# Kernel tuning notes

Measured on AMD Instinct MI355X. Metric: run time of the kernel, lower is better.

The kernel has to match this reference:

```python
import jax, jax.numpy as jnp
import numpy as np
from jax.ops import segment_sum

N_USERS = 100_000
N_ITEMS = 200_000
D = 64
NNZ = 5_000_000
GNN_LAYERS = 2


def setup_inputs() -> dict:
    key = jax.random.key(0)
    k0, k1, k2, k3, k4 = jax.random.split(key, 5)
    # Embedding tables (xavier-ish scale)
    user_emb = jax.random.normal(k0, (N_USERS, D), jnp.float32) * 0.1
    item_emb = jax.random.normal(k1, (N_ITEMS, D), jnp.float32) * 0.1
    # Sparse normalized bipartite adjacency adj_norm [n_users, n_items] in COO form
    adj_vals = jax.random.uniform(k2, (NNZ,), jnp.float32)
    adj_rows = jax.random.randint(k3, (NNZ,), 0, N_USERS, jnp.int32)
    adj_cols = jax.random.randint(k4, (NNZ,), 0, N_ITEMS, jnp.int32)
    return {
        "user_emb": user_emb,
        "item_emb": item_emb,
        "adj_vals": adj_vals,
        "adj_rows": adj_rows,
        "adj_cols": adj_cols,
    }


def reference(user_emb, item_emb, adj_vals, adj_rows, adj_cols):
    """Student_LightGCL.forward with is_test=True.

    NormLayer with mode 'None' is identity. Then gnn_layer rounds of
    bipartite sparse propagation:
      Z_u = adj_norm   @ E_i   (spmm -> gather + segment_sum over users)
      Z_i = adj_norm.T @ E_u
    Output: mean over layer-0..L embeddings for users and items.
    """
    E_u, E_i = user_emb, item_emb
    sum_u, sum_i = E_u, E_i
    for _ in range(GNN_LAYERS):
        # Z_u[r] = sum_{e: rows[e]==r} vals[e] * E_i[cols[e]]
        Z_u = segment_sum(adj_vals[:, None] * E_i[adj_cols], adj_rows,
                          num_segments=N_USERS)
        Z_i = segment_sum(adj_vals[:, None] * E_u[adj_rows], adj_cols,
                          num_segments=N_ITEMS)
        E_u, E_i = Z_u, Z_i
        sum_u = sum_u + E_u
        sum_i = sum_i + E_i
    inv = 1.0 / (GNN_LAYERS + 1)
    return sum_u * inv, sum_i * inv
```

## Files before the change

kernel.cpp:

```cpp
#include <hip/hip_runtime.h>


constexpr int D = 64;
constexpr int RPB = 64;
constexpr int ACC = 32;
constexpr int NBMAX = 5120;
constexpr int REF_CAP = 4000;
constexpr int PASSB_EDGES = 8192;

static __device__ __forceinline__ unsigned short f32_to_bf16(float f) {
    unsigned u = __float_as_uint(f);
    unsigned r = u + 0x7FFFu + ((u >> 16) & 1u);
    return (unsigned short)(r >> 16);
}
static __device__ __forceinline__ float bf16_lo(unsigned g) {
    return __uint_as_float(g << 16);
}
static __device__ __forceinline__ float bf16_hi(unsigned g) {
    return __uint_as_float(g & 0xFFFF0000u);
}


__global__ __launch_bounds__(1024) void bucket_hist(
    const int* __restrict__ rows, const int* __restrict__ cols,
    int* __restrict__ bktCnt, int nu, int nnz, int NB) {
    __shared__ int cnt[NBMAX];
    for (int i = threadIdx.x; i < NB; i += blockDim.x) cnt[i] = 0;
    __syncthreads();
    int stride = gridDim.x * blockDim.x;
    for (int e = blockIdx.x * blockDim.x + threadIdx.x; e < nnz; e += stride) {
        atomicAdd(&cnt[rows[e] >> 6], 1);
        atomicAdd(&cnt[(nu + cols[e]) >> 6], 1);
    }
    __syncthreads();
    for (int i = threadIdx.x; i < NB; i += blockDim.x)
        if (cnt[i]) atomicAdd(&bktCnt[i], cnt[i]);
}

__global__ void scan_buckets(const int* __restrict__ bktCnt,
                             int* __restrict__ bktBase, int* __restrict__ bktCur,
                             int NB, int total) {
    __shared__ int tsum[256];
    int t = threadIdx.x;
    const int IT = (NB + 255) / 256;
    int v[20];
    int s = 0;
    for (int k = 0; k < IT; k++) {
        int i = t * IT + k;
        v[k] = (i < NB) ? bktCnt[i] : 0;
        s += v[k];
    }
    tsum[t] = s;
    __syncthreads();
    for (int off = 1; off < 256; off <<= 1) {
        int x = (t >= off) ? tsum[t - off] : 0;
        __syncthreads();
        tsum[t] += x;
        __syncthreads();
    }
    int excl = (t > 0) ? tsum[t - 1] : 0;
    for (int k = 0; k < IT; k++) {
        int i = t * IT + k;
        if (i < NB) { bktBase[i] = excl; bktCur[i] = excl; excl += v[k]; }
    }
    if (t == 255) bktBase[NB] = total;
}

__global__ __launch_bounds__(512) void pass_bucket(
    const float* __restrict__ vals, const int* __restrict__ rows,
    const int* __restrict__ cols, int* __restrict__ bktCur,
    int2* __restrict__ tmp, int nu, int nnz, int NB) {
    __shared__ int cnt[NBMAX];
    for (int i = threadIdx.x; i < NB; i += 512) cnt[i] = 0;
    __syncthreads();
    int base = blockIdx.x * PASSB_EDGES;
    for (int k = 0; k < PASSB_EDGES / 512; k++) {
        int e = base + k * 512 + threadIdx.x;
        if (e < nnz) {
            atomicAdd(&cnt[rows[e] >> 6], 1);
            atomicAdd(&cnt[(nu + cols[e]) >> 6], 1);
        }
    }
    __syncthreads();
    for (int i = threadIdx.x; i < NB; i += 512) {
        int c = cnt[i];
        if (c) cnt[i] = atomicAdd(&bktCur[i], c);
    }
    __syncthreads();
    for (int k = 0; k < PASSB_EDGES / 512; k++) {
        int e = base + k * 512 + threadIdx.x;
        if (e < nnz) {
            int r = rows[e], c = cols[e];
            int iv = __float_as_int(vals[e]);
            int gi = nu + c;
            int p1 = atomicAdd(&cnt[r >> 6], 1);
            tmp[p1] = make_int2(((r & 63) << 19) | gi, iv);
            int p2 = atomicAdd(&cnt[gi >> 6], 1);
            tmp[p2] = make_int2(((gi & 63) << 19) | r, iv);
        }
    }
}

__global__ __launch_bounds__(512) void refine_kernel(
    int2* __restrict__ tmp, const int* __restrict__ bktBase,
    int* __restrict__ rowStart, int NB) {
    __shared__ int2 stage[REF_CAP];
    __shared__ int h[RPB], cur[RPB];
    int b = blockIdx.x;
    int beg = bktBase[b], end = bktBase[b + 1];
    int n = end - beg;
    int t = threadIdx.x;
    if (t == 0 && b == NB - 1) rowStart[(size_t)NB * RPB] = end;
    if (t < RPB) h[t] = 0;
    __syncthreads();
    if (n <= REF_CAP) {
        for (int e = t; e < n; e += 512) {
            int2 v = tmp[beg + e];
            stage[e] = v;
            atomicAdd(&h[(v.x >> 19) & (RPB - 1)], 1);
        }
        __syncthreads();
        int myc = (t < RPB) ? h[t] : 0;
        for (int off = 1; off < RPB; off <<= 1) {
            int x = 0;
            if (t < RPB && t >= off) x = h[t - off];
            __syncthreads();
            if (t < RPB) h[t] += x;
            __syncthreads();
        }
        if (t < RPB) {
            int excl = beg + h[t] - myc;
            cur[t] = excl;
            rowStart[(size_t)b * RPB + t] = excl;
        }
        __syncthreads();
        for (int e = t; e < n; e += 512) {
            int2 v = stage[e];
            int p = atomicAdd(&cur[(v.x >> 19) & (RPB - 1)], 1);
            tmp[p] = v;
        }
    } else {
        if (t < RPB) rowStart[(size_t)b * RPB + t] = (t == 0) ? -(beg + 1) : 0;
    }
}

__global__ void convert_e0(const float* __restrict__ Eu,
                           const float* __restrict__ Ei,
                           unsigned short* __restrict__ Ecat,
                           long long nuD, long long nD) {
    long long stride = (long long)gridDim.x * blockDim.x * 4;
    for (long long i = ((long long)blockIdx.x * blockDim.x + threadIdx.x) * 4;
         i < nD; i += stride) {
        const float* src = (i < nuD) ? (Eu + i) : (Ei + (i - nuD));
        float4 f = *(const float4*)src;
        unsigned short o0 = f32_to_bf16(f.x), o1 = f32_to_bf16(f.y);
        unsigned short o2 = f32_to_bf16(f.z), o3 = f32_to_bf16(f.w);
        *(uint2*)(Ecat + i) =
            make_uint2(((unsigned)o1 << 16) | o0, ((unsigned)o3 << 16) | o2);
    }
}

template <bool FUSE>
__global__ __launch_bounds__(256, 8) void accum7_kernel(
    const int2* __restrict__ tmp, const int* __restrict__ bktBase,
    const int* __restrict__ rowStart,
    const unsigned short* __restrict__ gsrc,
    const float* __restrict__ Eu0, const float* __restrict__ Ei0,
    const unsigned short* __restrict__ Z1,
    unsigned short* __restrict__ Zout,
    float* __restrict__ out,
    int nu, int nR) {
    int b = blockIdx.x;
    int w = threadIdx.x >> 6, lane = threadIdx.x & 63;
    int q = lane >> 4, m = lane & 15;
    int rb64 = (b * ACC) >> 6;
    int bEnd = bktBase[rb64 + 1];
    int rb0 = rowStart[(size_t)rb64 << 6];
    bool sorted = (rb0 >= 0);
    const uint2* gp = (const uint2*)gsrc + m;

    for (int k = 0; k < 8; k += 2) {
        int grA = b * ACC + (w << 3) + k;
        if (grA >= nR) break;
        bool hasB = (grA + 1) < nR;

        float a0 = 0.f, a1 = 0.f, a2 = 0.f, a3 = 0.f;
        float b0 = 0.f, b1 = 0.f, b2 = 0.f, b3 = 0.f;

        if (sorted) {
            int eA0 = rowStart[grA], eA1 = rowStart[grA + 1];
            int eB0 = eA1;
            int eB1 = hasB ? (((grA & 63) == 62) ? bEnd : rowStart[grA + 2])
                           : eB0;
            int nA = eA1 - eA0, nB = eB1 - eB0;
            int iters = ((nA > nB ? nA : nB) + 3) >> 2;
            int eA = eA0 + q, eB = eB0 + q;

            int2 sAc = tmp[eA], sBc = tmp[eB];
            int2 sAn = tmp[eA + 4], sBn = tmp[eB + 4];
            bool okA = eA < eA1, okB = eB < eB1;
            uint2 gAc = gp[(okA ? (sAc.x & 0x7FFFF) : 0) << 4];
            uint2 gBc = gp[(okB ? (sBc.x & 0x7FFFF) : 0) << 4];
            float vAc = okA ? __int_as_float(sAc.y) : 0.f;
            float vBc = okB ? __int_as_float(sBc.y) : 0.f;

            for (int i = 0; i < iters; i++) {
                int2 sAn2 = tmp[eA + 8];
                int2 sBn2 = tmp[eB + 8];
                bool okA1 = (eA + 4) < eA1;
                bool okB1 = (eB + 4) < eB1;
                uint2 gAn = gp[(okA1 ? (sAn.x & 0x7FFFF) : 0) << 4];
                uint2 gBn = gp[(okB1 ? (sBn.x & 0x7FFFF) : 0) << 4];
                float vAn = okA1 ? __int_as_float(sAn.y) : 0.f;
                float vBn = okB1 ? __int_as_float(sBn.y) : 0.f;

                a0 += vAc * bf16_lo(gAc.x); a1 += vAc * bf16_hi(gAc.x);
                a2 += vAc * bf16_lo(gAc.y); a3 += vAc * bf16_hi(gAc.y);
                b0 += vBc * bf16_lo(gBc.x); b1 += vBc * bf16_hi(gBc.x);
                b2 += vBc * bf16_lo(gBc.y); b3 += vBc * bf16_hi(gBc.y);

                sAn = sAn2; sBn = sBn2;
                gAc = gAn;  gBc = gBn;
                vAc = vAn;  vBc = vBn;
                eA += 4; eB += 4;
            }
        } else {
            int beg = -(rb0 + 1);
            int n = bEnd - beg;
            int iters = (n + 3) >> 2;
            int e = beg + q;
            int rlA = grA & 63;
            for (int i = 0; i < iters; i++) {
                int2 s = tmp[e];
                int rl = (s.x >> 19) & 63;
                bool in = e < bEnd;
                bool okA = in && (rl == rlA);
                bool okB = in && hasB && (rl == rlA + 1);
                int rx = (okA | okB) ? (s.x & 0x7FFFF) : 0;
                float vA = okA ? __int_as_float(s.y) : 0.f;
                float vB = okB ? __int_as_float(s.y) : 0.f;
                uint2 g = gp[rx << 4];
                a0 += vA * bf16_lo(g.x); a1 += vA * bf16_hi(g.x);
                a2 += vA * bf16_lo(g.y); a3 += vA * bf16_hi(g.y);
                b0 += vB * bf16_lo(g.x); b1 += vB * bf16_hi(g.x);
                b2 += vB * bf16_lo(g.y); b3 += vB * bf16_hi(g.y);
                e += 4;
            }
        }

        a0 += __shfl_xor(a0, 16, 64); a0 += __shfl_xor(a0, 32, 64);
        a1 += __shfl_xor(a1, 16, 64); a1 += __shfl_xor(a1, 32, 64);
        a2 += __shfl_xor(a2, 16, 64); a2 += __shfl_xor(a2, 32, 64);
        a3 += __shfl_xor(a3, 16, 64); a3 += __shfl_xor(a3, 32, 64);
        b0 += __shfl_xor(b0, 16, 64); b0 += __shfl_xor(b0, 32, 64);
        b1 += __shfl_xor(b1, 16, 64); b1 += __shfl_xor(b1, 32, 64);
        b2 += __shfl_xor(b2, 16, 64); b2 += __shfl_xor(b2, 32, 64);
        b3 += __shfl_xor(b3, 16, 64); b3 += __shfl_xor(b3, 32, 64);

        int wr = (q == 0) ? grA : ((q == 1 && hasB) ? grA + 1 : -1);
        if (wr >= 0) {
            float r0 = (q == 0) ? a0 : b0;
            float r1 = (q == 0) ? a1 : b1;
            float r2 = (q == 0) ? a2 : b2;
            float r3 = (q == 0) ? a3 : b3;
            long long o = (long long)wr * D + m * 4;
            if (!FUSE) {
                unsigned p0 = ((unsigned)f32_to_bf16(r1) << 16) | f32_to_bf16(r0);
                unsigned p1 = ((unsigned)f32_to_bf16(r3) << 16) | f32_to_bf16(r2);
                *(uint2*)(Zout + o) = make_uint2(p0, p1);
            } else {
                const float* e0p = (wr < nu)
                    ? (Eu0 + o) : (Ei0 + o - (long long)nu * D);
                float4 e0 = *(const float4*)e0p;
                uint2 z = *(const uint2*)(Z1 + o);
                const float inv3 = 1.f / 3.f;
                float4 ov;
                ov.x = (e0.x + bf16_lo(z.x) + r0) * inv3;
                ov.y = (e0.y + bf16_hi(z.x) + r1) * inv3;
                ov.z = (e0.z + bf16_lo(z.y) + r2) * inv3;
                ov.w = (e0.w + bf16_hi(z.y) + r3) * inv3;
                *(float4*)(out + o) = ov;
            }
        }
    }
}


__global__ void spmm_edge(const float* __restrict__ vals,
                          const int* __restrict__ rows,
                          const int* __restrict__ cols,
                          const float* __restrict__ Eu,
                          const float* __restrict__ Ei,
                          float* __restrict__ Zu, float* __restrict__ Zi,
                          float scale, int nnz) {
    long long gid = (long long)blockIdx.x * blockDim.x + threadIdx.x;
    if (gid >= (long long)nnz * D) return;
    int e = (int)(gid >> 6);
    int d = (int)(gid & 63);
    float v = vals[e] * scale;
    long long r = rows[e];
    long long c = cols[e];
    atomicAdd(&Zu[r * D + d], v * Ei[c * D + d]);
    atomicAdd(&Zi[c * D + d], v * Eu[r * D + d]);
}

__global__ void combine_kernel(const float* __restrict__ E0,
                               const float* __restrict__ Z1,
                               float* __restrict__ out, long long n4) {
    long long i = (long long)blockIdx.x * blockDim.x + threadIdx.x;
    if (i >= n4) return;
    const float4 a = reinterpret_cast<const float4*>(E0)[i];
    const float4 b = reinterpret_cast<const float4*>(Z1)[i];
    const float inv3 = 1.0f / 3.0f;
    float4 o;
    o.x = (a.x + b.x) * inv3;
    o.y = (a.y + b.y) * inv3;
    o.z = (a.z + b.z) * inv3;
    o.w = (a.w + b.w) * inv3;
    reinterpret_cast<float4*>(out)[i] = o;
}


static inline size_t align256(size_t x) { return (x + 255) & ~(size_t)255; }

extern "C" void kernel_launch(void* const* d_in, const int* in_sizes, int n_in,
                              void* d_out, int out_size, void* d_ws, size_t ws_size,
                              hipStream_t stream) {
    const float* user_emb = (const float*)d_in[0];
    const float* item_emb = (const float*)d_in[1];
    const float* vals     = (const float*)d_in[2];
    const int*   rows     = (const int*)d_in[3];
    const int*   cols     = (const int*)d_in[4];

    const int nu  = in_sizes[0] / D;
    const int ni  = in_sizes[1] / D;
    const int nnz = in_sizes[2];
    const int nR  = nu + ni;
    const int NB  = (nR + RPB - 1) / RPB;

    float* out = (float*)d_out;

    size_t off = 0;
    size_t o_tmp  = off; off += align256(((size_t)2 * nnz + 32) * sizeof(int2));
    size_t o_E    = off; off += align256((size_t)nR * D * sizeof(unsigned short));
    size_t o_Z1   = off; off += align256((size_t)nR * D * sizeof(unsigned short));
    size_t o_cnt  = off; off += align256((size_t)(NB + 1) * sizeof(int));
    size_t o_base = off; off += align256((size_t)(NB + 2) * sizeof(int));
    size_t o_cur  = off; off += align256((size_t)(NB + 1) * sizeof(int));
    size_t o_row  = off; off += align256(((size_t)NB * RPB + 1) * sizeof(int));
    size_t needed = off;

    bool fits19 = (nR < (1 << 19));

    if (ws_size >= needed && NB <= NBMAX && fits19) {
        char* w = (char*)d_ws;
        int2*           tmp      = (int2*)(w + o_tmp);
        unsigned short* Ecat     = (unsigned short*)(w + o_E);
        unsigned short* Z1bf     = (unsigned short*)(w + o_Z1);
        int*            bktCnt   = (int*)(w + o_cnt);
        int*            bktBase  = (int*)(w + o_base);
        int*            bktCur   = (int*)(w + o_cur);
        int*            rowStart = (int*)(w + o_row);

        hipMemsetAsync(bktCnt, 0, (size_t)NB * sizeof(int), stream);

        bucket_hist<<<512, 1024, 0, stream>>>(rows, cols, bktCnt, nu, nnz, NB);
        scan_buckets<<<1, 256, 0, stream>>>(bktCnt, bktBase, bktCur, NB, 2 * nnz);

        unsigned gB = (unsigned)((nnz + PASSB_EDGES - 1) / PASSB_EDGES);
        pass_bucket<<<gB, 512, 0, stream>>>(vals, rows, cols, bktCur, tmp,
                                            nu, nnz, NB);
        refine_kernel<<<NB, 512, 0, stream>>>(tmp, bktBase, rowStart, NB);

        long long nD = (long long)nR * D;
        long long nuD = (long long)nu * D;
        unsigned gC = (unsigned)((nD / 4 + 255) / 256);
        if (gC > 4096) gC = 4096;
        convert_e0<<<gC, 256, 0, stream>>>(user_emb, item_emb, Ecat, nuD, nD);

        unsigned gA = (unsigned)((nR + ACC - 1) / ACC);
        accum7_kernel<false><<<gA, 256, 0, stream>>>(
            tmp, bktBase, rowStart, Ecat, nullptr, nullptr, nullptr, Z1bf,
            nullptr, nu, nR);
        accum7_kernel<true><<<gA, 256, 0, stream>>>(
            tmp, bktBase, rowStart, Z1bf, user_emb, item_emb, Z1bf, nullptr,
            out, nu, nR);
    } else {
        float* Zu1 = (float*)d_ws;
        float* Zi1 = Zu1 + (size_t)nu * D;
        float* out_u = out;
        float* out_i = out + (size_t)nu * D;
        hipMemsetAsync(d_ws, 0, (size_t)nR * D * sizeof(float), stream);

        const int threads = 256;
        long long tot = (long long)nnz * D;
        unsigned blocks = (unsigned)((tot + threads - 1) / threads);

        spmm_edge<<<blocks, threads, 0, stream>>>(vals, rows, cols, user_emb,
                                                  item_emb, Zu1, Zi1, 1.0f, nnz);
        long long nu4 = (long long)nu * D / 4;
        long long ni4 = (long long)ni * D / 4;
        combine_kernel<<<(unsigned)((nu4 + 255) / 256), 256, 0, stream>>>(
            user_emb, Zu1, out_u, nu4);
        combine_kernel<<<(unsigned)((ni4 + 255) / 256), 256, 0, stream>>>(
            item_emb, Zi1, out_i, ni4);
        spmm_edge<<<blocks, threads, 0, stream>>>(vals, rows, cols, Zu1, Zi1,
                                                  out_u, out_i, 1.0f / 3.0f, nnz);
    }
}
```

Before: 780.4 us.

## Fuse per-bucket refine sort with first-layer SpMM accumulation from shared memory

The separate refine kernel is folded into a new accum_sort_l1 kernel. It sorts each 64-row bucket in shared memory using an index permutation, writes the sorted edges back for layer 2, and computes the layer-1 aggregation directly from the staged edges instead of re-reading them from global memory in a separate launch. pass_bucket also moves from 512 to 1024 threads per block. The costs are one fewer launch and one fewer global read of the edge list, traded against heavier per-block shared memory use (lower occupancy) and 512-thread blocks doing the gather work.

```diff
diff --git a/kernel.cpp b/kernel.cpp
--- a/kernel.cpp
+++ b/kernel.cpp
@@ -66,29 +66,29 @@
     if (t == 255) bktBase[NB] = total;
 }
 
-__global__ __launch_bounds__(512) void pass_bucket(
+__global__ __launch_bounds__(1024) void pass_bucket(
     const float* __restrict__ vals, const int* __restrict__ rows,
     const int* __restrict__ cols, int* __restrict__ bktCur,
     int2* __restrict__ tmp, int nu, int nnz, int NB) {
     __shared__ int cnt[NBMAX];
-    for (int i = threadIdx.x; i < NB; i += 512) cnt[i] = 0;
+    for (int i = threadIdx.x; i < NB; i += 1024) cnt[i] = 0;
     __syncthreads();
     int base = blockIdx.x * PASSB_EDGES;
-    for (int k = 0; k < PASSB_EDGES / 512; k++) {
-        int e = base + k * 512 + threadIdx.x;
+    for (int k = 0; k < PASSB_EDGES / 1024; k++) {
+        int e = base + k * 1024 + threadIdx.x;
         if (e < nnz) {
             atomicAdd(&cnt[rows[e] >> 6], 1);
             atomicAdd(&cnt[(nu + cols[e]) >> 6], 1);
         }
     }
     __syncthreads();
-    for (int i = threadIdx.x; i < NB; i += 512) {
+    for (int i = threadIdx.x; i < NB; i += 1024) {
         int c = cnt[i];
         if (c) cnt[i] = atomicAdd(&bktCur[i], c);
     }
     __syncthreads();
-    for (int k = 0; k < PASSB_EDGES / 512; k++) {
-        int e = base + k * 512 + threadIdx.x;
+    for (int k = 0; k < PASSB_EDGES / 1024; k++) {
+        int e = base + k * 1024 + threadIdx.x;
         if (e < nnz) {
             int r = rows[e], c = cols[e];
             int iv = __float_as_int(vals[e]);
@@ -98,49 +98,6 @@
             int p2 = atomicAdd(&cnt[gi >> 6], 1);
             tmp[p2] = make_int2(((gi & 63) << 19) | r, iv);
         }
-    }
-}
-
-__global__ __launch_bounds__(512) void refine_kernel(
-    int2* __restrict__ tmp, const int* __restrict__ bktBase,
-    int* __restrict__ rowStart, int NB) {
-    __shared__ int2 stage[REF_CAP];
-    __shared__ int h[RPB], cur[RPB];
-    int b = blockIdx.x;
-    int beg = bktBase[b], end = bktBase[b + 1];
-    int n = end - beg;
-    int t = threadIdx.x;
-    if (t == 0 && b == NB - 1) rowStart[(size_t)NB * RPB] = end;
-    if (t < RPB) h[t] = 0;
-    __syncthreads();
-    if (n <= REF_CAP) {
-        for (int e = t; e < n; e += 512) {
-            int2 v = tmp[beg + e];
-            stage[e] = v;
-            atomicAdd(&h[(v.x >> 19) & (RPB - 1)], 1);
-        }
-        __syncthreads();
-        int myc = (t < RPB) ? h[t] : 0;
-        for (int off = 1; off < RPB; off <<= 1) {
-            int x = 0;
-            if (t < RPB && t >= off) x = h[t - off];
-            __syncthreads();
-            if (t < RPB) h[t] += x;
-            __syncthreads();
-        }
-        if (t < RPB) {
-            int excl = beg + h[t] - myc;
-            cur[t] = excl;
-            rowStart[(size_t)b * RPB + t] = excl;
-        }
-        __syncthreads();
-        for (int e = t; e < n; e += 512) {
-            int2 v = stage[e];
-            int p = atomicAdd(&cur[(v.x >> 19) & (RPB - 1)], 1);
-            tmp[p] = v;
-        }
-    } else {
-        if (t < RPB) rowStart[(size_t)b * RPB + t] = (t == 0) ? -(beg + 1) : 0;
     }
 }
 
@@ -160,14 +117,175 @@
     }
 }
 
-template <bool FUSE>
+__global__ __launch_bounds__(512) void accum_sort_l1(
+    int2* __restrict__ tmp, const int* __restrict__ bktBase,
+    int* __restrict__ rowStart,
+    const unsigned short* __restrict__ gsrc,
+    unsigned short* __restrict__ Zout,
+    int nu, int nR) {
+    __shared__ int2 stage[REF_CAP];
+    __shared__ unsigned short idx[REF_CAP];
+    __shared__ int h[RPB], cur[RPB], rs[RPB + 1];
+    int b = blockIdx.x;
+    int beg = bktBase[b], end = bktBase[b + 1];
+    int n = end - beg;
+    int t = threadIdx.x;
+    if (t < RPB) h[t] = 0;
+    if (t == 0) { stage[0] = make_int2(0, 0); idx[0] = 0; }
+    __syncthreads();
+
+    int w = t >> 6, lane = t & 63;
+    int q = lane >> 4, m = lane & 15;
+    const uint2* gp = (const uint2*)gsrc + m;
+
+    if (n <= REF_CAP) {
+        for (int e = t; e < n; e += 512) {
+            int2 v = tmp[beg + e];
+            stage[e] = v;
+            atomicAdd(&h[(v.x >> 19) & (RPB - 1)], 1);
+        }
+        __syncthreads();
+        int myc = (t < RPB) ? h[t] : 0;
+        for (int off = 1; off < RPB; off <<= 1) {
+            int x = 0;
+            if (t < RPB && t >= off) x = h[t - off];
+            __syncthreads();
+            if (t < RPB) h[t] += x;
+            __syncthreads();
+        }
+        if (t < RPB) {
+            int excl = h[t] - myc;
+            cur[t] = excl;
+            rs[t] = excl;
+            rowStart[(size_t)b * RPB + t] = beg + excl;
+        }
+        if (t == 0) rs[RPB] = n;
+        __syncthreads();
+        for (int e = t; e < n; e += 512) {
+            int2 v = stage[e];
+            int p = atomicAdd(&cur[(v.x >> 19) & (RPB - 1)], 1);
+            idx[p] = (unsigned short)e;
+        }
+        __syncthreads();
+        for (int e = t; e < n; e += 512) tmp[beg + e] = stage[idx[e]];
+
+        for (int k = 0; k < 8; k += 2) {
+            int rlA = (w << 3) + k;
+            int grA = b * RPB + rlA;
+            if (grA >= nR) break;
+            bool hasB = (grA + 1) < nR;
+            int eA0 = rs[rlA], eA1 = rs[rlA + 1];
+            int eB0 = eA1;
+            int eB1 = hasB ? rs[rlA + 2] : eA1;
+            int nA = eA1 - eA0, nB = eB1 - eB0;
+            int iters = ((nA > nB ? nA : nB) + 3) >> 2;
+
+            float a0 = 0.f, a1 = 0.f, a2 = 0.f, a3 = 0.f;
+            float b0 = 0.f, b1 = 0.f, b2 = 0.f, b3 = 0.f;
+            int eA = eA0 + q, eB = eB0 + q;
+
+            bool okA = eA < eA1, okB = eB < eB1;
+            int2 sA = stage[idx[okA ? eA : 0]];
+            int2 sB = stage[idx[okB ? eB : 0]];
+            uint2 gA = gp[(okA ? (sA.x & 0x7FFFF) : 0) << 4];
+            uint2 gB = gp[(okB ? (sB.x & 0x7FFFF) : 0) << 4];
+            float vA = okA ? __int_as_float(sA.y) : 0.f;
+            float vB = okB ? __int_as_float(sB.y) : 0.f;
+
+            for (int i = 0; i < iters; i++) {
+                bool okA1 = (eA + 4) < eA1, okB1 = (eB + 4) < eB1;
+                int2 sAn = stage[idx[okA1 ? eA + 4 : 0]];
+                int2 sBn = stage[idx[okB1 ? eB + 4 : 0]];
+
+                a0 += vA * bf16_lo(gA.x); a1 += vA * bf16_hi(gA.x);
+                a2 += vA * bf16_lo(gA.y); a3 += vA * bf16_hi(gA.y);
+                b0 += vB * bf16_lo(gB.x); b1 += vB * bf16_hi(gB.x);
+                b2 += vB * bf16_lo(gB.y); b3 += vB * bf16_hi(gB.y);
+
+                gA = gp[(okA1 ? (sAn.x & 0x7FFFF) : 0) << 4];
+                gB = gp[(okB1 ? (sBn.x & 0x7FFFF) : 0) << 4];
+                vA = okA1 ? __int_as_float(sAn.y) : 0.f;
+                vB = okB1 ? __int_as_float(sBn.y) : 0.f;
+                eA += 4; eB += 4;
+            }
+
+            a0 += __shfl_xor(a0, 16, 64); a0 += __shfl_xor(a0, 32, 64);
+            a1 += __shfl_xor(a1, 16, 64); a1 += __shfl_xor(a1, 32, 64);
+            a2 += __shfl_xor(a2, 16, 64); a2 += __shfl_xor(a2, 32, 64);
+            a3 += __shfl_xor(a3, 16, 64); a3 += __shfl_xor(a3, 32, 64);
+            b0 += __shfl_xor(b0, 16, 64); b0 += __shfl_xor(b0, 32, 64);
+            b1 += __shfl_xor(b1, 16, 64); b1 += __shfl_xor(b1, 32, 64);
+            b2 += __shfl_xor(b2, 16, 64); b2 += __shfl_xor(b2, 32, 64);
+            b3 += __shfl_xor(b3, 16, 64); b3 += __shfl_xor(b3, 32, 64);
+
+            int wr = (q == 0) ? grA : ((q == 1 && hasB) ? grA + 1 : -1);
+            if (wr >= 0) {
+                float r0 = (q == 0) ? a0 : b0;
+                float r1 = (q == 0) ? a1 : b1;
+                float r2 = (q == 0) ? a2 : b2;
+                float r3 = (q == 0) ? a3 : b3;
+                long long o = (long long)wr * D + m * 4;
+                unsigned p0 = ((unsigned)f32_to_bf16(r1) << 16) | f32_to_bf16(r0);
+                unsigned p1 = ((unsigned)f32_to_bf16(r3) << 16) | f32_to_bf16(r2);
+                *(uint2*)(Zout + o) = make_uint2(p0, p1);
+            }
+        }
+    } else {
+        if (t < RPB) rowStart[(size_t)b * RPB + t] = (t == 0) ? -(beg + 1) : 0;
+        __syncthreads();
+        for (int k = 0; k < 8; k += 2) {
+            int rlA = (w << 3) + k;
+            int grA = b * RPB + rlA;
+            if (grA >= nR) break;
+            bool hasB = (grA + 1) < nR;
+            float a0 = 0.f, a1 = 0.f, a2 = 0.f, a3 = 0.f;
+            float b0 = 0.f, b1 = 0.f, b2 = 0.f, b3 = 0.f;
+            int iters = (n + 3) >> 2;
+            int e = beg + q;
+            for (int i = 0; i < iters; i++) {
+                int2 s = (e < end) ? tmp[e] : make_int2(0, 0);
+                int rl = (s.x >> 19) & (RPB - 1);
+                bool okA = (e < end) && (rl == rlA);
+                bool okB = (e < end) && hasB && (rl == rlA + 1);
+                int rx = (okA | okB) ? (s.x & 0x7FFFF) : 0;
+                float vA = okA ? __int_as_float(s.y) : 0.f;
+                float vB = okB ? __int_as_float(s.y) : 0.f;
+                uint2 g = gp[rx << 4];
+                a0 += vA * bf16_lo(g.x); a1 += vA * bf16_hi(g.x);
+                a2 += vA * bf16_lo(g.y); a3 += vA * bf16_hi(g.y);
+                b0 += vB * bf16_lo(g.x); b1 += vB * bf16_hi(g.x);
+                b2 += vB * bf16_lo(g.y); b3 += vB * bf16_hi(g.y);
+                e += 4;
+            }
+            a0 += __shfl_xor(a0, 16, 64); a0 += __shfl_xor(a0, 32, 64);
+            a1 += __shfl_xor(a1, 16, 64); a1 += __shfl_xor(a1, 32, 64);
+            a2 += __shfl_xor(a2, 16, 64); a2 += __shfl_xor(a2, 32, 64);
+            a3 += __shfl_xor(a3, 16, 64); a3 += __shfl_xor(a3, 32, 64);
+            b0 += __shfl_xor(b0, 16, 64); b0 += __shfl_xor(b0, 32, 64);
+            b1 += __shfl_xor(b1, 16, 64); b1 += __shfl_xor(b1, 32, 64);
+            b2 += __shfl_xor(b2, 16, 64); b2 += __shfl_xor(b2, 32, 64);
+            b3 += __shfl_xor(b3, 16, 64); b3 += __shfl_xor(b3, 32, 64);
+            int wr = (q == 0) ? grA : ((q == 1 && hasB) ? grA + 1 : -1);
+            if (wr >= 0) {
+                float r0 = (q == 0) ? a0 : b0;
+                float r1 = (q == 0) ? a1 : b1;
+                float r2 = (q == 0) ? a2 : b2;
+                float r3 = (q == 0) ? a3 : b3;
+                long long o = (long long)wr * D + m * 4;
+                unsigned p0 = ((unsigned)f32_to_bf16(r1) << 16) | f32_to_bf16(r0);
+                unsigned p1 = ((unsigned)f32_to_bf16(r3) << 16) | f32_to_bf16(r2);
+                *(uint2*)(Zout + o) = make_uint2(p0, p1);
+            }
+        }
+    }
+}
+
 __global__ __launch_bounds__(256, 8) void accum7_kernel(
     const int2* __restrict__ tmp, const int* __restrict__ bktBase,
     const int* __restrict__ rowStart,
     const unsigned short* __restrict__ gsrc,
     const float* __restrict__ Eu0, const float* __restrict__ Ei0,
     const unsigned short* __restrict__ Z1,
-    unsigned short* __restrict__ Zout,
     float* __restrict__ out,
     int nu, int nR) {
     int b = blockIdx.x;
@@ -264,23 +382,17 @@
             float r2 = (q == 0) ? a2 : b2;
             float r3 = (q == 0) ? a3 : b3;
             long long o = (long long)wr * D + m * 4;
-            if (!FUSE) {
-                unsigned p0 = ((unsigned)f32_to_bf16(r1) << 16) | f32_to_bf16(r0);
-                unsigned p1 = ((unsigned)f32_to_bf16(r3) << 16) | f32_to_bf16(r2);
-                *(uint2*)(Zout + o) = make_uint2(p0, p1);
-            } else {
-                const float* e0p = (wr < nu)
-                    ? (Eu0 + o) : (Ei0 + o - (long long)nu * D);
-                float4 e0 = *(const float4*)e0p;
-                uint2 z = *(const uint2*)(Z1 + o);
-                const float inv3 = 1.f / 3.f;
-                float4 ov;
-                ov.x = (e0.x + bf16_lo(z.x) + r0) * inv3;
-                ov.y = (e0.y + bf16_hi(z.x) + r1) * inv3;
-                ov.z = (e0.z + bf16_lo(z.y) + r2) * inv3;
-                ov.w = (e0.w + bf16_hi(z.y) + r3) * inv3;
-                *(float4*)(out + o) = ov;
-            }
+            const float* e0p = (wr < nu)
+                ? (Eu0 + o) : (Ei0 + o - (long long)nu * D);
+            float4 e0 = *(const float4*)e0p;
+            uint2 z = *(const uint2*)(Z1 + o);
+            const float inv3 = 1.f / 3.f;
+            float4 ov;
+            ov.x = (e0.x + bf16_lo(z.x) + r0) * inv3;
+            ov.y = (e0.y + bf16_hi(z.x) + r1) * inv3;
+            ov.z = (e0.z + bf16_lo(z.y) + r2) * inv3;
+            ov.w = (e0.w + bf16_hi(z.y) + r3) * inv3;
+            *(float4*)(out + o) = ov;
         }
     }
 }
@@ -368,9 +480,8 @@
         scan_buckets<<<1, 256, 0, stream>>>(bktCnt, bktBase, bktCur, NB, 2 * nnz);
 
         unsigned gB = (unsigned)((nnz + PASSB_EDGES - 1) / PASSB_EDGES);
-        pass_bucket<<<gB, 512, 0, stream>>>(vals, rows, cols, bktCur, tmp,
-                                            nu, nnz, NB);
-        refine_kernel<<<NB, 512, 0, stream>>>(tmp, bktBase, rowStart, NB);
+        pass_bucket<<<gB, 1024, 0, stream>>>(vals, rows, cols, bktCur, tmp,
+                                             nu, nnz, NB);
 
         long long nD = (long long)nR * D;
         long long nuD = (long long)nu * D;
@@ -378,12 +489,12 @@
         if (gC > 4096) gC = 4096;
         convert_e0<<<gC, 256, 0, stream>>>(user_emb, item_emb, Ecat, nuD, nD);
 
+        accum_sort_l1<<<NB, 512, 0, stream>>>(tmp, bktBase, rowStart, Ecat,
+                                              Z1bf, nu, nR);
+
         unsigned gA = (unsigned)((nR + ACC - 1) / ACC);
-        accum7_kernel<false><<<gA, 256, 0, stream>>>(
-            tmp, bktBase, rowStart, Ecat, nullptr, nullptr, nullptr, Z1bf,
-            nullptr, nu, nR);
-        accum7_kernel<true><<<gA, 256, 0, stream>>>(
-            tmp, bktBase, rowStart, Z1bf, user_emb, item_emb, Z1bf, nullptr,
+        accum7_kernel<<<gA, 256, 0, stream>>>(
+            tmp, bktBase, rowStart, Z1bf, user_emb, item_emb, Z1bf,
             out, nu, nR);
     } else {
         float* Zu1 = (float*)d_ws;
```

Measured after the change: 704.7 us. 9.7% less time.
